# Kernel optimization log

Measured on AMD Instinct MI355X. Metric: run time of the kernel, lower is better.

Reference implementation:

```python
import jax, jax.numpy as jnp
import numpy as np

INDIM = 128
OUTDIM = 256
GRID = 16


def setup_inputs() -> dict:
    key = jax.random.key(0)
    kx, kc = jax.random.split(key)
    x = jax.random.normal(kx, (32768, INDIM), dtype=jnp.float32)
    # fouriercoeffs: (2, outdim, indim, gridsize), init randn / (sqrt(indim)*sqrt(gridsize))
    fouriercoeffs = jax.random.normal(kc, (2, OUTDIM, INDIM, GRID), dtype=jnp.float32) / (
        np.sqrt(INDIM) * np.sqrt(GRID)
    )
    bias = jnp.zeros((1, OUTDIM), dtype=jnp.float32)
    return {"x": x, "fouriercoeffs": fouriercoeffs, "bias": bias}


def reference(x, fouriercoeffs, bias):
    orig_shape = x.shape
    x2 = x.reshape(-1, INDIM)  # (N, indim)
    k = jnp.arange(1, GRID + 1, dtype=x2.dtype)  # (gridsize,)
    x_scaled = x2[:, :, None] * k  # (N, indim, gridsize)
    y = (
        jnp.einsum("nig,oig->no", jnp.cos(x_scaled), fouriercoeffs[0])
        + jnp.einsum("nig,oig->no", jnp.sin(x_scaled), fouriercoeffs[1])
        + bias
    )
    return y.reshape(*orig_shape[:-1], OUTDIM)
```

## Files before the change

### kernel.cpp

```cpp
#include <hip/hip_runtime.h>
#include <cstdint>

#define IN_DIM   128
#define OUT_DIM  256
#define NROWS    32768
#define NSTEPS   32

typedef unsigned short u16;
typedef __attribute__((ext_vector_type(8)))  __bf16 bf16x8;
typedef __attribute__((ext_vector_type(16))) float  f32x16;
typedef __attribute__((ext_vector_type(4)))  float  f32x4v;

__global__ __launch_bounds__(256) void kan_prep(const float* __restrict__ C,
                                                u16* __restrict__ Bpack) {
    const int o = threadIdx.x;
    const int i = blockIdx.x;
    const int t = blockIdx.y;
    const float* src = C + (((size_t)(t * OUT_DIM + o) * IN_DIM + i) * 16);
    bf16x8 lo = {}, hi = {};
#pragma unroll
    for (int g = 0; g < 8; ++g) {
        lo[g] = (__bf16)src[g];
        hi[g] = (__bf16)src[8 + g];
    }
    const int ko = i * 4 + t * 2;
    bf16x8* dst = (bf16x8*)Bpack;
    dst[(size_t)ko * OUT_DIM + o]       = lo;
    dst[(size_t)(ko + 1) * OUT_DIM + o] = hi;
}

__global__ __launch_bounds__(64, 1) void kan_gemm(const float* __restrict__ x,
                                                  const u16* __restrict__ Bpack,
                                                  const float* __restrict__ bias,
                                                  float* __restrict__ out) {
    const int lane = threadIdx.x;
    const int la31 = lane & 31;
    const int gh   = lane >> 5;
    const int bid  = blockIdx.x;
    const int wn   = bid & 1;
    const int m0   = (bid >> 1) * 64;

    f32x16 vz;
#pragma unroll
    for (int r = 0; r < 16; ++r) vz[r] = 0.f;
    f32x16 acc[2][4] = {{vz, vz, vz, vz}, {vz, vz, vz, vz}};

    const bf16x8* Bv = (const bf16x8*)Bpack;
    const int bcol = wn * 128 + la31;

    const float* xr0 = x + (size_t)(m0 + la31) * IN_DIM;
    const float* xr1 = xr0 + (size_t)32 * IN_DIM;

    auto chain = [&](float xv, bf16x8& afc, bf16x8& afs) {
        float s1, c1;
        __sincosf(xv, &s1, &c1);
        const float t2 = 2.f * c1;
        bf16x8 qc0 = {}, qc1 = {}, qs0 = {}, qs1 = {};
        float cp = c1, sp = s1;
        float cc = t2 * c1 - 1.f, sc = t2 * s1;
        qc0[0] = (__bf16)cp;  qs0[0] = (__bf16)sp;
        qc0[1] = (__bf16)cc;  qs0[1] = (__bf16)sc;
#pragma unroll
        for (int g = 3; g <= 16; ++g) {
            const float cn = t2 * cc - cp;
            const float sn = t2 * sc - sp;
            cp = cc; sp = sc; cc = cn; sc = sn;
            const int idx = g - 1;
            if (idx < 8) { qc0[idx] = (__bf16)cc;      qs0[idx] = (__bf16)sc; }
            else         { qc1[idx - 8] = (__bf16)cc;  qs1[idx - 8] = (__bf16)sc; }
        }
        afc = gh ? qc1 : qc0;
        afs = gh ? qs1 : qs0;
    };

    f32x4v xa = *(const f32x4v*)(xr0);
    f32x4v xb = *(const f32x4v*)(xr1);

    for (int kt = 0; kt < NSTEPS; ++kt) {
        const int ktn = (kt + 1) & (NSTEPS - 1);
        const f32x4v xa_n = *(const f32x4v*)(xr0 + ktn * 4);
        const f32x4v xb_n = *(const f32x4v*)(xr1 + ktn * 4);

#pragma unroll
        for (int i = 0; i < 4; ++i) {
            const size_t koc = (size_t)((kt * 4 + i) * 4 + gh);
            bf16x8 bgc[4], bgs[4];
#pragma unroll
            for (int fn = 0; fn < 4; ++fn) {
                bgc[fn] = Bv[koc * OUT_DIM + bcol + fn * 32];
                bgs[fn] = Bv[(koc + 2) * OUT_DIM + bcol + fn * 32];
            }

            bf16x8 afc0, afs0, afc1, afs1;
            chain(xa[i], afc0, afs0);
            chain(xb[i], afc1, afs1);

#pragma unroll
            for (int fn = 0; fn < 4; ++fn) {
                acc[0][fn] = __builtin_amdgcn_mfma_f32_32x32x16_bf16(afc0, bgc[fn], acc[0][fn], 0, 0, 0);
                acc[1][fn] = __builtin_amdgcn_mfma_f32_32x32x16_bf16(afc1, bgc[fn], acc[1][fn], 0, 0, 0);
            }
#pragma unroll
            for (int fn = 0; fn < 4; ++fn) {
                acc[0][fn] = __builtin_amdgcn_mfma_f32_32x32x16_bf16(afs0, bgs[fn], acc[0][fn], 0, 0, 0);
                acc[1][fn] = __builtin_amdgcn_mfma_f32_32x32x16_bf16(afs1, bgs[fn], acc[1][fn], 0, 0, 0);
            }
        }
        xa = xa_n;
        xb = xb_n;
    }

#pragma unroll
    for (int fn = 0; fn < 4; ++fn) {
        const int col = bcol + fn * 32;
        const float bv = bias[col];
#pragma unroll
        for (int fm = 0; fm < 2; ++fm) {
            const int rbase = m0 + fm * 32 + 4 * gh;
#pragma unroll
            for (int r = 0; r < 16; ++r) {
                const int row = rbase + (r & 3) + 8 * (r >> 2);
                out[(size_t)row * OUT_DIM + col] = acc[fm][fn][r] + bv;
            }
        }
    }
}

extern "C" void kernel_launch(void* const* d_in, const int* in_sizes, int n_in,
                              void* d_out, int out_size, void* d_ws, size_t ws_size,
                              hipStream_t stream) {
    const float* x    = (const float*)d_in[0];
    const float* fc   = (const float*)d_in[1];
    const float* bias = (const float*)d_in[2];
    float* out        = (float*)d_out;
    u16* Bpack        = (u16*)d_ws;

    kan_prep<<<dim3(IN_DIM, 2), OUT_DIM, 0, stream>>>(fc, Bpack);
    kan_gemm<<<dim3(NROWS / 64 * 2), 64, 0, stream>>>(x, Bpack, bias, out);
}
```

Measured before the change: 95.63 us.

## Split K across two waves per block with LDS reduction

Each block now runs two waves, each covering half of the input dimension, and the partial accumulators are combined through shared memory before the bias-add and store. This doubles the number of resident waves, to better hide MFMA and sin/cos chain latency in a kernel that previously ran one wave per block. It adds a 32KB LDS reduction, a block barrier, and serialised output stores by one wave.

```diff
diff --git a/kernel.cpp b/kernel.cpp
--- a/kernel.cpp
+++ b/kernel.cpp
@@ -4,7 +4,7 @@
 #define IN_DIM   128
 #define OUT_DIM  256
 #define NROWS    32768
-#define NSTEPS   32
+#define NSTEPS_L 16
 
 typedef unsigned short u16;
 typedef __attribute__((ext_vector_type(8)))  __bf16 bf16x8;
@@ -29,11 +29,15 @@
     dst[(size_t)(ko + 1) * OUT_DIM + o] = hi;
 }
 
-__global__ __launch_bounds__(64, 1) void kan_gemm(const float* __restrict__ x,
-                                                  const u16* __restrict__ Bpack,
-                                                  const float* __restrict__ bias,
-                                                  float* __restrict__ out) {
-    const int lane = threadIdx.x;
+__global__ __launch_bounds__(128, 2) void kan_gemm(const float* __restrict__ x,
+                                                   const u16* __restrict__ Bpack,
+                                                   const float* __restrict__ bias,
+                                                   float* __restrict__ out) {
+    __shared__ __align__(16) float red[64 * 128];
+
+    const int tid  = threadIdx.x;
+    const int lane = tid & 63;
+    const int kh   = tid >> 6;
     const int la31 = lane & 31;
     const int gh   = lane >> 5;
     const int bid  = blockIdx.x;
@@ -48,7 +52,7 @@
     const bf16x8* Bv = (const bf16x8*)Bpack;
     const int bcol = wn * 128 + la31;
 
-    const float* xr0 = x + (size_t)(m0 + la31) * IN_DIM;
+    const float* xr0 = x + (size_t)(m0 + la31) * IN_DIM + kh * 64;
     const float* xr1 = xr0 + (size_t)32 * IN_DIM;
 
     auto chain = [&](float xv, bf16x8& afc, bf16x8& afs) {
@@ -76,14 +80,14 @@
     f32x4v xa = *(const f32x4v*)(xr0);
     f32x4v xb = *(const f32x4v*)(xr1);
 
-    for (int kt = 0; kt < NSTEPS; ++kt) {
-        const int ktn = (kt + 1) & (NSTEPS - 1);
+    for (int kt = 0; kt < NSTEPS_L; ++kt) {
+        const int ktn = (kt + 1) & (NSTEPS_L - 1);
         const f32x4v xa_n = *(const f32x4v*)(xr0 + ktn * 4);
         const f32x4v xb_n = *(const f32x4v*)(xr1 + ktn * 4);
 
 #pragma unroll
         for (int i = 0; i < 4; ++i) {
-            const size_t koc = (size_t)((kt * 4 + i) * 4 + gh);
+            const size_t koc = (size_t)((kh * 64 + kt * 4 + i) * 4 + gh);
             bf16x8 bgc[4], bgs[4];
 #pragma unroll
             for (int fn = 0; fn < 4; ++fn) {
@@ -110,17 +114,37 @@
         xb = xb_n;
     }
 
+    if (kh == 1) {
 #pragma unroll
-    for (int fn = 0; fn < 4; ++fn) {
-        const int col = bcol + fn * 32;
-        const float bv = bias[col];
+        for (int fn = 0; fn < 4; ++fn) {
+            const int colL = fn * 32 + la31;
 #pragma unroll
-        for (int fm = 0; fm < 2; ++fm) {
-            const int rbase = m0 + fm * 32 + 4 * gh;
+            for (int fm = 0; fm < 2; ++fm) {
+                const int rbase = fm * 32 + 4 * gh;
 #pragma unroll
-            for (int r = 0; r < 16; ++r) {
-                const int row = rbase + (r & 3) + 8 * (r >> 2);
-                out[(size_t)row * OUT_DIM + col] = acc[fm][fn][r] + bv;
+                for (int r = 0; r < 16; ++r) {
+                    const int row = rbase + (r & 3) + 8 * (r >> 2);
+                    red[row * 128 + colL] = acc[fm][fn][r];
+                }
+            }
+        }
+    }
+    __syncthreads();
+    if (kh == 0) {
+#pragma unroll
+        for (int fn = 0; fn < 4; ++fn) {
+            const int colL = fn * 32 + la31;
+            const int col  = wn * 128 + colL;
+            const float bv = bias[col];
+#pragma unroll
+            for (int fm = 0; fm < 2; ++fm) {
+                const int rbase = fm * 32 + 4 * gh;
+#pragma unroll
+                for (int r = 0; r < 16; ++r) {
+                    const int row = rbase + (r & 3) + 8 * (r >> 2);
+                    out[(size_t)(m0 + row) * OUT_DIM + col] =
+                        acc[fm][fn][r] + red[row * 128 + colL] + bv;
+                }
             }
         }
     }
@@ -136,5 +160,5 @@
     u16* Bpack        = (u16*)d_ws;
 
     kan_prep<<<dim3(IN_DIM, 2), OUT_DIM, 0, stream>>>(fc, Bpack);
-    kan_gemm<<<dim3(NROWS / 64 * 2), 64, 0, stream>>>(x, Bpack, bias, out);
+    kan_gemm<<<dim3(NROWS / 64 * 2), 128, 0, stream>>>(x, Bpack, bias, out);
 }
```

Measured after the change: 110.6 us. 1.16x slower.

## Split output columns across four waves and share chain via lane shuffle

Applied to the files above, without the earlier changes.

Each wave now covers 64 output columns instead of 128, so the grid doubles and each wave holds half as many accumulators. The sin/cos Chebyshev chain, which was computed twice per lane (once for each 32-row half), is now computed once per lane for its own row. The other half of the A fragment is fetched from the opposite half-wave with a cross-lane shuffle. Launch bounds move to 2 waves per SIMD. In exchange, the trig chain is recomputed across twice as many waves for the same rows, B is reloaded more often overall, and the shuffles add cost.

```diff
diff --git a/kernel.cpp b/kernel.cpp
--- a/kernel.cpp
+++ b/kernel.cpp
@@ -29,7 +29,15 @@
     dst[(size_t)(ko + 1) * OUT_DIM + o] = hi;
 }
 
-__global__ __launch_bounds__(64, 1) void kan_gemm(const float* __restrict__ x,
+__device__ inline bf16x8 swap32(bf16x8 v) {
+    union { bf16x8 h; int i[4]; } u;
+    u.h = v;
+#pragma unroll
+    for (int j = 0; j < 4; ++j) u.i[j] = __shfl_xor(u.i[j], 32, 64);
+    return u.h;
+}
+
+__global__ __launch_bounds__(64, 2) void kan_gemm(const float* __restrict__ x,
                                                   const u16* __restrict__ Bpack,
                                                   const float* __restrict__ bias,
                                                   float* __restrict__ out) {
@@ -37,81 +45,78 @@
     const int la31 = lane & 31;
     const int gh   = lane >> 5;
     const int bid  = blockIdx.x;
-    const int wn   = bid & 1;
-    const int m0   = (bid >> 1) * 64;
+    const int wn   = bid & 3;
+    const int m0   = (bid >> 2) * 64;
 
     f32x16 vz;
 #pragma unroll
     for (int r = 0; r < 16; ++r) vz[r] = 0.f;
-    f32x16 acc[2][4] = {{vz, vz, vz, vz}, {vz, vz, vz, vz}};
+    f32x16 acc[2][2] = {{vz, vz}, {vz, vz}};
 
     const bf16x8* Bv = (const bf16x8*)Bpack;
-    const int bcol = wn * 128 + la31;
+    const int bcol = wn * 64 + la31;
 
-    const float* xr0 = x + (size_t)(m0 + la31) * IN_DIM;
-    const float* xr1 = xr0 + (size_t)32 * IN_DIM;
+    const float* xr = x + (size_t)(m0 + la31 + 32 * gh) * IN_DIM;
 
-    auto chain = [&](float xv, bf16x8& afc, bf16x8& afs) {
-        float s1, c1;
-        __sincosf(xv, &s1, &c1);
-        const float t2 = 2.f * c1;
-        bf16x8 qc0 = {}, qc1 = {}, qs0 = {}, qs1 = {};
-        float cp = c1, sp = s1;
-        float cc = t2 * c1 - 1.f, sc = t2 * s1;
-        qc0[0] = (__bf16)cp;  qs0[0] = (__bf16)sp;
-        qc0[1] = (__bf16)cc;  qs0[1] = (__bf16)sc;
-#pragma unroll
-        for (int g = 3; g <= 16; ++g) {
-            const float cn = t2 * cc - cp;
-            const float sn = t2 * sc - sp;
-            cp = cc; sp = sc; cc = cn; sc = sn;
-            const int idx = g - 1;
-            if (idx < 8) { qc0[idx] = (__bf16)cc;      qs0[idx] = (__bf16)sc; }
-            else         { qc1[idx - 8] = (__bf16)cc;  qs1[idx - 8] = (__bf16)sc; }
-        }
-        afc = gh ? qc1 : qc0;
-        afs = gh ? qs1 : qs0;
-    };
-
-    f32x4v xa = *(const f32x4v*)(xr0);
-    f32x4v xb = *(const f32x4v*)(xr1);
+    f32x4v xa = *(const f32x4v*)(xr);
 
     for (int kt = 0; kt < NSTEPS; ++kt) {
         const int ktn = (kt + 1) & (NSTEPS - 1);
-        const f32x4v xa_n = *(const f32x4v*)(xr0 + ktn * 4);
-        const f32x4v xb_n = *(const f32x4v*)(xr1 + ktn * 4);
+        const f32x4v xa_n = *(const f32x4v*)(xr + ktn * 4);
 
 #pragma unroll
         for (int i = 0; i < 4; ++i) {
             const size_t koc = (size_t)((kt * 4 + i) * 4 + gh);
-            bf16x8 bgc[4], bgs[4];
+            bf16x8 bgc[2], bgs[2];
 #pragma unroll
-            for (int fn = 0; fn < 4; ++fn) {
+            for (int fn = 0; fn < 2; ++fn) {
                 bgc[fn] = Bv[koc * OUT_DIM + bcol + fn * 32];
                 bgs[fn] = Bv[(koc + 2) * OUT_DIM + bcol + fn * 32];
             }
 
-            bf16x8 afc0, afs0, afc1, afs1;
-            chain(xa[i], afc0, afs0);
-            chain(xb[i], afc1, afs1);
+            bf16x8 qc0 = {}, qc1 = {}, qs0 = {}, qs1 = {};
+            {
+                float s1, c1;
+                __sincosf(xa[i], &s1, &c1);
+                const float t2 = 2.f * c1;
+                float cp = c1, sp = s1;
+                float cc = t2 * c1 - 1.f, sc = t2 * s1;
+                qc0[0] = (__bf16)cp;  qs0[0] = (__bf16)sp;
+                qc0[1] = (__bf16)cc;  qs0[1] = (__bf16)sc;
+#pragma unroll
+                for (int g = 3; g <= 16; ++g) {
+                    const float cn = t2 * cc - cp;
+                    const float sn = t2 * sc - sp;
+                    cp = cc; sp = sc; cc = cn; sc = sn;
+                    const int idx = g - 1;
+                    if (idx < 8) { qc0[idx] = (__bf16)cc;      qs0[idx] = (__bf16)sc; }
+                    else         { qc1[idx - 8] = (__bf16)cc;  qs1[idx - 8] = (__bf16)sc; }
+                }
+            }
+
+            const bf16x8 recv_c = swap32(gh ? qc0 : qc1);
+            const bf16x8 recv_s = swap32(gh ? qs0 : qs1);
+            const bf16x8 afc0 = gh ? recv_c : qc0;
+            const bf16x8 afc1 = gh ? qc1 : recv_c;
+            const bf16x8 afs0 = gh ? recv_s : qs0;
+            const bf16x8 afs1 = gh ? qs1 : recv_s;
 
 #pragma unroll
-            for (int fn = 0; fn < 4; ++fn) {
+            for (int fn = 0; fn < 2; ++fn) {
                 acc[0][fn] = __builtin_amdgcn_mfma_f32_32x32x16_bf16(afc0, bgc[fn], acc[0][fn], 0, 0, 0);
                 acc[1][fn] = __builtin_amdgcn_mfma_f32_32x32x16_bf16(afc1, bgc[fn], acc[1][fn], 0, 0, 0);
             }
 #pragma unroll
-            for (int fn = 0; fn < 4; ++fn) {
+            for (int fn = 0; fn < 2; ++fn) {
                 acc[0][fn] = __builtin_amdgcn_mfma_f32_32x32x16_bf16(afs0, bgs[fn], acc[0][fn], 0, 0, 0);
                 acc[1][fn] = __builtin_amdgcn_mfma_f32_32x32x16_bf16(afs1, bgs[fn], acc[1][fn], 0, 0, 0);
             }
         }
         xa = xa_n;
-        xb = xb_n;
     }
 
 #pragma unroll
-    for (int fn = 0; fn < 4; ++fn) {
+    for (int fn = 0; fn < 2; ++fn) {
         const int col = bcol + fn * 32;
         const float bv = bias[col];
 #pragma unroll
@@ -136,5 +141,5 @@
     u16* Bpack        = (u16*)d_ws;
 
     kan_prep<<<dim3(IN_DIM, 2), OUT_DIM, 0, stream>>>(fc, Bpack);
-    kan_gemm<<<dim3(NROWS / 64 * 2), 64, 0, stream>>>(x, Bpack, bias, out);
+    kan_gemm<<<dim3(NROWS / 64 * 4), 64, 0, stream>>>(x, Bpack, bias, out);
 }
```

After: 125.4 us. 31.1% more time.
